# Kernel optimization log

Hardware: AMD Instinct MI355X
Metric: run time of the kernel (lower is better)

## Reference

```python
import jax, jax.numpy as jnp
import numpy as np

B, I, H = 4096, 2048, 2048


def setup_inputs() -> dict:
    key = jax.random.key(0)
    k1, k2, k3, k4, k5 = jax.random.split(key, 5)
    return {
        "x": jax.random.normal(k1, (B, I), dtype=jnp.float32),
        "coefficients": jax.random.normal(k2, (I, H), dtype=jnp.float32) * 0.1,
        "amplitude_an": jax.random.normal(k3, (1, I, H), dtype=jnp.float32) * 0.1,
        "amplitude_bn": jax.random.normal(k4, (1, I, H), dtype=jnp.float32) * 0.1,
        "bias": jax.random.normal(k5, (1, I), dtype=jnp.float32),
    }


def reference(x, coefficients, amplitude_an, amplitude_bn, bias):
    # phase[b,h] = x[b,:] @ coefficients[:,h]  (same matmul done per-sample in torch loop)
    phase = x @ coefficients  # [B, H]
    num_harmonics = coefficients.shape[1]
    # sum over harmonics of an[i,h]*cos(phase[b,h]) + bn[i,h]*sin(phase[b,h])
    gain = (
        jnp.einsum("bh,ih->bi", jnp.cos(phase), amplitude_an[0])
        + jnp.einsum("bh,ih->bi", jnp.sin(phase), amplitude_bn[0])
        + num_harmonics * bias  # bias added per-harmonic before the sum over H
    )
    return gain  # [B, I]
```

## Files before the change

### kernel.cpp

```cpp
#include <hip/hip_runtime.h>
#include <hip/hip_bf16.h>

#define B_DIM 4096
#define I_DIM 2048
#define H_DIM 2048

typedef unsigned char u8;
typedef unsigned short u16;
typedef unsigned int u32;
typedef __attribute__((ext_vector_type(4))) float f32x4;
typedef __attribute__((ext_vector_type(4))) int i32x4;
typedef __attribute__((ext_vector_type(8))) int i32x8;

__device__ __forceinline__ void gload_lds16(const void* g, void* l) {
  __builtin_amdgcn_global_load_lds(
      (const __attribute__((address_space(1))) void*)g,
      (__attribute__((address_space(3))) void*)l, 16, 0, 0);
}

__device__ __forceinline__ u32 f2fp4(float v, float inv_scale) {
  const float a = fabsf(v) * inv_scale;
  u32 m = (u32)(a > 0.25f) + (u32)(a > 0.75f) + (u32)(a > 1.25f) +
          (u32)(a > 1.75f) + (u32)(a > 2.5f) + (u32)(a > 3.5f) + (u32)(a > 5.0f);
  return ((__float_as_uint(v) >> 31) << 3) | m;
}

__global__ void convert_ew(const float* __restrict__ x, const float* __restrict__ an,
                           const float* __restrict__ bn, u16* __restrict__ xf4,
                           u32* __restrict__ ab4) {
  const long NX4 = (long)B_DIM * I_DIM / 4;
  const long NA4 = (long)I_DIM * H_DIM / 4;
  const long total = NX4 + NA4;
  for (long t = (long)blockIdx.x * blockDim.x + threadIdx.x; t < total;
       t += (long)gridDim.x * blockDim.x) {
    if (t < NX4) {
      float4 v = *(const float4*)(x + t * 4);
      u32 b0 = f2fp4(v.x, 1.f) | (f2fp4(v.y, 1.f) << 4);
      u32 b1 = f2fp4(v.z, 1.f) | (f2fp4(v.w, 1.f) << 4);
      xf4[t] = (u16)(b0 | (b1 << 8));
    } else {
      long p = (t - NX4) * 4;
      float4 va = *(const float4*)(an + p);
      float4 vb = *(const float4*)(bn + p);
      u32 b0 = f2fp4(va.x, 8.f) | (f2fp4(vb.x, 8.f) << 4);
      u32 b1 = f2fp4(va.y, 8.f) | (f2fp4(vb.y, 8.f) << 4);
      u32 b2 = f2fp4(va.z, 8.f) | (f2fp4(vb.z, 8.f) << 4);
      u32 b3 = f2fp4(va.w, 8.f) | (f2fp4(vb.w, 8.f) << 4);
      ab4[p >> 2] = b0 | (b1 << 8) | (b2 << 16) | (b3 << 24);
    }
  }
}

__global__ void transpose_conv(const float* __restrict__ c, u16* __restrict__ ct4) {
  __shared__ float tile[32][33];
  const int i0 = blockIdx.y * 32;
  const int h0 = blockIdx.x * 32;
  const int tid = threadIdx.x;
  const int tx = tid & 31;
  const int ty = tid >> 5;
  for (int r = ty; r < 32; r += 8)
    tile[r][tx] = c[(long)(i0 + r) * H_DIM + (h0 + tx)];
  __syncthreads();
  const int hl = tid >> 3;
  const int q = (tid & 7) * 4;
  u32 w = f2fp4(tile[q + 0][hl], 8.f) | (f2fp4(tile[q + 1][hl], 8.f) << 4) |
          (f2fp4(tile[q + 2][hl], 8.f) << 8) | (f2fp4(tile[q + 3][hl], 8.f) << 12);
  ct4[(long)(h0 + hl) * (I_DIM / 4) + ((i0 + q) >> 2)] = (u16)w;
}

__device__ __forceinline__ void stage_tile(const char* Ab, const char* Bb, long kbyte,
                                           long lda, long ldb, char* Adst, char* Bdst,
                                           int tid) {
#pragma unroll
  for (int i = 0; i < 4; ++i) {
    const int o = i * 4096 + tid * 16;
    const int row = o >> 7;
    const int ls = ((((o >> 4) & 7) ^ (row & 7)) << 4);
    gload_lds16(Ab + (long)row * lda + kbyte + ls, Adst + o);
  }
#pragma unroll
  for (int i = 0; i < 4; ++i) {
    const int o = i * 4096 + tid * 16;
    const int row = o >> 7;
    const int ls = ((((o >> 4) & 7) ^ (row & 7)) << 4);
    gload_lds16(Bb + (long)row * ldb + kbyte + ls, Bdst + o);
  }
}

__device__ __forceinline__ i32x4 frag_ld16(const char* S, int row, int slot) {
  return *(const i32x4*)(S + row * 128 + ((slot ^ (row & 7)) << 4));
}

template <int SCALE_A, int SCALE_B>
__device__ __forceinline__ void gemm_kloop_fp4(const char* __restrict__ A,
                                               const char* __restrict__ Bt,
                                               int rowA0, int colB0, long Kbytes,
                                               char* smem, f32x4 acc[4][4]) {
  const int tid = threadIdx.x;
  const int lane = tid & 63;
  const int wid = tid >> 6;
  const int wr = wid >> 1, wc = wid & 1;
  const long lda = Kbytes, ldb = Kbytes;
  const char* Ab = A + (long)rowA0 * lda;
  const char* Bb = Bt + (long)colB0 * ldb;
  const int arow = wr * 64 + (lane & 15);
  const int brow = wc * 64 + (lane & 15);
  const int g = lane >> 4;
  const int nt = (int)(Kbytes >> 7);
  char* AsB = smem;
  char* BsB = smem + 32768;

  stage_tile(Ab, Bb, 0, lda, ldb, AsB, BsB, tid);

  for (int t = 0; t < nt; ++t) {
    const int cur = (t & 1) << 14;
    asm volatile("s_waitcnt vmcnt(0)" ::: "memory");
    __builtin_amdgcn_sched_barrier(0);
    __builtin_amdgcn_s_barrier();
    __builtin_amdgcn_sched_barrier(0);

    i32x8 af[2][4], bfr[2][4];
#pragma unroll
    for (int s = 0; s < 2; ++s)
#pragma unroll
      for (int m = 0; m < 4; ++m) {
        *(i32x4*)&af[s][m]  = frag_ld16(AsB + cur, arow + m * 16, s * 4 + g);
        *(i32x4*)&bfr[s][m] = frag_ld16(BsB + cur, brow + m * 16, s * 4 + g);
      }
    if (t + 1 < nt)
      stage_tile(Ab, Bb, (long)(t + 1) * 128, lda, ldb,
                 AsB + (cur ^ 16384), BsB + (cur ^ 16384), tid);
    __builtin_amdgcn_sched_barrier(0);
    asm volatile("s_waitcnt lgkmcnt(0)" ::: "memory");
    __builtin_amdgcn_sched_barrier(0);

    __builtin_amdgcn_s_setprio(1);
#pragma unroll
    for (int s = 0; s < 2; ++s)
#pragma unroll
      for (int m = 0; m < 4; ++m)
#pragma unroll
        for (int n = 0; n < 4; ++n)
          acc[m][n] = __builtin_amdgcn_mfma_scale_f32_16x16x128_f8f6f4(
              af[s][m], bfr[s][n], acc[m][n], 4, 4, 0, SCALE_A, 0, SCALE_B);
    __builtin_amdgcn_s_setprio(0);
    __builtin_amdgcn_sched_barrier(0);
  }
}

__device__ __forceinline__ void tile_xy(int GX, int& bx, int& by) {
  const int bid = blockIdx.x;
  const int id = (bid & 7) * 64 + (bid >> 3);
  bx = id & (GX - 1);
  by = id / GX;
}

__global__ __launch_bounds__(256) void gemm_phase(const char* __restrict__ xf4,
                                                  const char* __restrict__ ct4,
                                                  u8* __restrict__ cs4) {
  __shared__ __align__(16) char smem[65536];
  int bx, by;
  tile_xy(16, bx, by);
  const int rowA0 = by * 128;
  const int colB0 = bx * 128;
  f32x4 acc[4][4];
#pragma unroll
  for (int m = 0; m < 4; ++m)
#pragma unroll
    for (int n = 0; n < 4; ++n)
#pragma unroll
      for (int j = 0; j < 4; ++j) acc[m][n][j] = 0.0f;

  gemm_kloop_fp4<0x7F7F7F7F, 0x7C7C7C7C>(xf4, ct4, rowA0, colB0, I_DIM / 2, smem, acc);

  const int lane = threadIdx.x & 63;
  const int wid = threadIdx.x >> 6;
  const int wr = wid >> 1, wc = wid & 1;
#pragma unroll
  for (int m = 0; m < 4; ++m) {
#pragma unroll
    for (int n = 0; n < 4; ++n) {
      const int col = colB0 + wc * 64 + n * 16 + (lane & 15);
#pragma unroll
      for (int j = 0; j < 4; ++j) {
        const int row = rowA0 + wr * 64 + m * 16 + (lane >> 4) * 4 + j;
        const float p = acc[m][n][j];
        const u32 b = f2fp4(__cosf(p), 4.f) | (f2fp4(__sinf(p), 4.f) << 4);
        cs4[(long)row * H_DIM + col] = (u8)b;
      }
    }
  }
}

__global__ __launch_bounds__(256) void gemm_gain(const char* __restrict__ cs4,
                                                 const char* __restrict__ ab4,
                                                 const float* __restrict__ bias,
                                                 float* __restrict__ out) {
  __shared__ __align__(16) char smem[65536];
  int bx, by;
  tile_xy(16, bx, by);
  const int rowA0 = by * 128;
  const int colB0 = bx * 128;
  f32x4 acc[4][4];
#pragma unroll
  for (int m = 0; m < 4; ++m)
#pragma unroll
    for (int n = 0; n < 4; ++n)
#pragma unroll
      for (int j = 0; j < 4; ++j) acc[m][n][j] = 0.0f;

  gemm_kloop_fp4<0x7D7D7D7D, 0x7C7C7C7C>(cs4, ab4, rowA0, colB0, H_DIM, smem, acc);

  const int lane = threadIdx.x & 63;
  const int wid = threadIdx.x >> 6;
  const int wr = wid >> 1, wc = wid & 1;
#pragma unroll
  for (int m = 0; m < 4; ++m) {
#pragma unroll
    for (int n = 0; n < 4; ++n) {
      const int col = colB0 + wc * 64 + n * 16 + (lane & 15);
      const float bv = 2048.0f * bias[col];
#pragma unroll
      for (int j = 0; j < 4; ++j) {
        const int row = rowA0 + wr * 64 + m * 16 + (lane >> 4) * 4 + j;
        out[(long)row * I_DIM + col] = acc[m][n][j] + bv;
      }
    }
  }
}

extern "C" void kernel_launch(void* const* d_in, const int* in_sizes, int n_in,
                              void* d_out, int out_size, void* d_ws, size_t ws_size,
                              hipStream_t stream) {
  const float* x     = (const float*)d_in[0];
  const float* coeff = (const float*)d_in[1];
  const float* an    = (const float*)d_in[2];
  const float* bn    = (const float*)d_in[3];
  const float* bias  = (const float*)d_in[4];
  float* out = (float*)d_out;

  char* ws = (char*)d_ws;
  char* xf4 = ws;
  char* ct4 = ws + (4L << 20);
  char* ab4 = ws + (8L << 20);
  u8*  cs4  = (u8*)(ws + (12L << 20));

  convert_ew<<<1024, 256, 0, stream>>>(x, an, bn, (u16*)xf4, (u32*)ab4);
  transpose_conv<<<dim3(H_DIM / 32, I_DIM / 32), 256, 0, stream>>>(coeff, (u16*)ct4);
  gemm_phase<<<512, 256, 0, stream>>>(xf4, ct4, cs4);
  gemm_gain<<<512, 256, 0, stream>>>((const char*)cs4, (const char*)ab4, bias, out);
}
```

Before: 66.40 us.

## Load A fragments directly from global into registers, stage only B in LDS

The FP4 GEMM k-loop now reads A-operand fragments straight from global memory into registers, double-buffered in two register arrays across an unrolled pair of iterations. Only the B tile still goes through LDS via global_load_lds. This halves LDS use per block (64KB to 32KB), which may allow more resident blocks, and removes the A LDS write/read traffic. In exchange, A loads are uncoalesced 16-byte per-lane global reads shared redundantly by the two waves with the same row offset, and register pressure rises.

New measurement: 96.33 us. 1.45x slower.

```diff
diff --git a/kernel.cpp b/kernel.cpp
--- a/kernel.cpp
+++ b/kernel.cpp
@@ -68,16 +68,8 @@
   ct4[(long)(h0 + hl) * (I_DIM / 4) + ((i0 + q) >> 2)] = (u16)w;
 }
 
-__device__ __forceinline__ void stage_tile(const char* Ab, const char* Bb, long kbyte,
-                                           long lda, long ldb, char* Adst, char* Bdst,
-                                           int tid) {
-#pragma unroll
-  for (int i = 0; i < 4; ++i) {
-    const int o = i * 4096 + tid * 16;
-    const int row = o >> 7;
-    const int ls = ((((o >> 4) & 7) ^ (row & 7)) << 4);
-    gload_lds16(Ab + (long)row * lda + kbyte + ls, Adst + o);
-  }
+__device__ __forceinline__ void stageB(const char* Bb, long kbyte, long ldb,
+                                       char* Bdst, int tid) {
 #pragma unroll
   for (int i = 0; i < 4; ++i) {
     const int o = i * 4096 + tid * 16;
@@ -91,60 +83,66 @@
   return *(const i32x4*)(S + row * 128 + ((slot ^ (row & 7)) << 4));
 }
 
-template <int SCALE_A, int SCALE_B>
+#define FS_ITER(CUR, NXT, t)                                                     \
+  {                                                                              \
+    asm volatile("s_waitcnt vmcnt(0)" ::: "memory");                             \
+    __builtin_amdgcn_sched_barrier(0);                                           \
+    __builtin_amdgcn_s_barrier();                                                \
+    __builtin_amdgcn_sched_barrier(0);                                           \
+    const char* Bs = BsB + (((t) & 1) << 14);                                    \
+    i32x8 bfr[8];                                                                \
+    _Pragma("unroll") for (int s = 0; s < 2; ++s)                                \
+      _Pragma("unroll") for (int n = 0; n < 4; ++n)                              \
+        *(i32x4*)&bfr[s * 4 + n] = frag_ld16(Bs, brow + n * 16, s * 4 + g);      \
+    if ((t) + 1 < nt) {                                                          \
+      const long kb = ((long)(t) + 1) * 128;                                     \
+      _Pragma("unroll") for (int s = 0; s < 2; ++s)                              \
+        _Pragma("unroll") for (int m = 0; m < 4; ++m)                            \
+          *(i32x4*)&NXT[s * 4 + m] =                                             \
+              *(const i32x4*)(Arow + (long)m * 16 * lda + kb + (s * 4 + g) * 16);\
+      stageB(Bb, kb, ldb, BsB + ((((t) + 1) & 1) << 14), tid);                   \
+    }                                                                            \
+    __builtin_amdgcn_sched_barrier(0);                                           \
+    asm volatile("s_waitcnt lgkmcnt(0)" ::: "memory");                           \
+    __builtin_amdgcn_sched_barrier(0);                                           \
+    __builtin_amdgcn_s_setprio(1);                                               \
+    _Pragma("unroll") for (int s = 0; s < 2; ++s)                                \
+      _Pragma("unroll") for (int m = 0; m < 4; ++m)                              \
+        _Pragma("unroll") for (int n = 0; n < 4; ++n)                            \
+          acc[m][n] = __builtin_amdgcn_mfma_scale_f32_16x16x128_f8f6f4(          \
+              CUR[s * 4 + m], bfr[s * 4 + n], acc[m][n], 4, 4, 0, SA, 0, SB);    \
+    __builtin_amdgcn_s_setprio(0);                                               \
+    __builtin_amdgcn_sched_barrier(0);                                           \
+  }
+
+template <int SA, int SB>
 __device__ __forceinline__ void gemm_kloop_fp4(const char* __restrict__ A,
                                                const char* __restrict__ Bt,
                                                int rowA0, int colB0, long Kbytes,
-                                               char* smem, f32x4 acc[4][4]) {
+                                               char* BsB, f32x4 acc[4][4]) {
   const int tid = threadIdx.x;
   const int lane = tid & 63;
   const int wid = tid >> 6;
   const int wr = wid >> 1, wc = wid & 1;
   const long lda = Kbytes, ldb = Kbytes;
-  const char* Ab = A + (long)rowA0 * lda;
   const char* Bb = Bt + (long)colB0 * ldb;
-  const int arow = wr * 64 + (lane & 15);
+  const char* Arow = A + (long)(rowA0 + wr * 64 + (lane & 15)) * lda;
   const int brow = wc * 64 + (lane & 15);
   const int g = lane >> 4;
   const int nt = (int)(Kbytes >> 7);
-  char* AsB = smem;
-  char* BsB = smem + 32768;
-
-  stage_tile(Ab, Bb, 0, lda, ldb, AsB, BsB, tid);
-
-  for (int t = 0; t < nt; ++t) {
-    const int cur = (t & 1) << 14;
-    asm volatile("s_waitcnt vmcnt(0)" ::: "memory");
-    __builtin_amdgcn_sched_barrier(0);
-    __builtin_amdgcn_s_barrier();
-    __builtin_amdgcn_sched_barrier(0);
-
-    i32x8 af[2][4], bfr[2][4];
-#pragma unroll
-    for (int s = 0; s < 2; ++s)
-#pragma unroll
-      for (int m = 0; m < 4; ++m) {
-        *(i32x4*)&af[s][m]  = frag_ld16(AsB + cur, arow + m * 16, s * 4 + g);
-        *(i32x4*)&bfr[s][m] = frag_ld16(BsB + cur, brow + m * 16, s * 4 + g);
-      }
-    if (t + 1 < nt)
-      stage_tile(Ab, Bb, (long)(t + 1) * 128, lda, ldb,
-                 AsB + (cur ^ 16384), BsB + (cur ^ 16384), tid);
-    __builtin_amdgcn_sched_barrier(0);
-    asm volatile("s_waitcnt lgkmcnt(0)" ::: "memory");
-    __builtin_amdgcn_sched_barrier(0);
-
-    __builtin_amdgcn_s_setprio(1);
-#pragma unroll
-    for (int s = 0; s < 2; ++s)
-#pragma unroll
-      for (int m = 0; m < 4; ++m)
-#pragma unroll
-        for (int n = 0; n < 4; ++n)
-          acc[m][n] = __builtin_amdgcn_mfma_scale_f32_16x16x128_f8f6f4(
-              af[s][m], bfr[s][n], acc[m][n], 4, 4, 0, SCALE_A, 0, SCALE_B);
-    __builtin_amdgcn_s_setprio(0);
-    __builtin_amdgcn_sched_barrier(0);
+
+  i32x8 afA[8], afB[8];
+#pragma unroll
+  for (int s = 0; s < 2; ++s)
+#pragma unroll
+    for (int m = 0; m < 4; ++m)
+      *(i32x4*)&afA[s * 4 + m] =
+          *(const i32x4*)(Arow + (long)m * 16 * lda + (s * 4 + g) * 16);
+  stageB(Bb, 0, ldb, BsB, tid);
+
+  for (int t = 0; t < nt; t += 2) {
+    FS_ITER(afA, afB, t);
+    FS_ITER(afB, afA, t + 1);
   }
 }
 
@@ -158,7 +156,7 @@
 __global__ __launch_bounds__(256) void gemm_phase(const char* __restrict__ xf4,
                                                   const char* __restrict__ ct4,
                                                   u8* __restrict__ cs4) {
-  __shared__ __align__(16) char smem[65536];
+  __shared__ __align__(16) char smem[32768];
   int bx, by;
   tile_xy(16, bx, by);
   const int rowA0 = by * 128;
@@ -196,7 +194,7 @@
                                                  const char* __restrict__ ab4,
                                                  const float* __restrict__ bias,
                                                  float* __restrict__ out) {
-  __shared__ __align__(16) char smem[65536];
+  __shared__ __align__(16) char smem[32768];
   int bx, by;
   tile_xy(16, bx, by);
   const int rowA0 = by * 128;
```

## Use 128x256 tiles with 8 waves and triple-buffered LDS prefetch

Applied to the files above, without the earlier changes.

Both FP4 GEMM kernels move from 128x128 tiles with 4 waves to 128x256 tiles with 8 waves (512 threads), giving 256 blocks, one per CU. The LDS pipeline goes from double to triple buffering with a prefetch distance of two K-tiles. A partial vmcnt wait lets the next tile's loads stay in flight while the current one is consumed. The aim is to hide global-load latency and reuse each A tile across more columns, at the cost of about 147KB of LDS and one block per CU, which leaves less latency hiding from co-resident blocks.

New measurement: 67.05 us. About the same (+1.0%).

```diff
diff --git a/kernel.cpp b/kernel.cpp
--- a/kernel.cpp
+++ b/kernel.cpp
@@ -68,22 +68,23 @@
   ct4[(long)(h0 + hl) * (I_DIM / 4) + ((i0 + q) >> 2)] = (u16)w;
 }
 
+#define NBUF 49152
+
 __device__ __forceinline__ void stage_tile(const char* Ab, const char* Bb, long kbyte,
-                                           long lda, long ldb, char* Adst, char* Bdst,
-                                           int tid) {
-#pragma unroll
-  for (int i = 0; i < 4; ++i) {
-    const int o = i * 4096 + tid * 16;
+                                           long lda, long ldb, char* buf, int tid) {
+#pragma unroll
+  for (int i = 0; i < 2; ++i) {
+    const int o = i * 8192 + tid * 16;
     const int row = o >> 7;
     const int ls = ((((o >> 4) & 7) ^ (row & 7)) << 4);
-    gload_lds16(Ab + (long)row * lda + kbyte + ls, Adst + o);
+    gload_lds16(Ab + (long)row * lda + kbyte + ls, buf + o);
   }
 #pragma unroll
   for (int i = 0; i < 4; ++i) {
-    const int o = i * 4096 + tid * 16;
+    const int o = i * 8192 + tid * 16;
     const int row = o >> 7;
     const int ls = ((((o >> 4) & 7) ^ (row & 7)) << 4);
-    gload_lds16(Bb + (long)row * ldb + kbyte + ls, Bdst + o);
+    gload_lds16(Bb + (long)row * ldb + kbyte + ls, buf + 16384 + o);
   }
 }
 
@@ -91,7 +92,7 @@
   return *(const i32x4*)(S + row * 128 + ((slot ^ (row & 7)) << 4));
 }
 
-template <int SCALE_A, int SCALE_B>
+template <int SA, int SB>
 __device__ __forceinline__ void gemm_kloop_fp4(const char* __restrict__ A,
                                                const char* __restrict__ Bt,
                                                int rowA0, int colB0, long Kbytes,
@@ -99,7 +100,8 @@
   const int tid = threadIdx.x;
   const int lane = tid & 63;
   const int wid = tid >> 6;
-  const int wr = wid >> 1, wc = wid & 1;
+  const int wr = wid >> 2;
+  const int wc = wid & 3;
   const long lda = Kbytes, ldb = Kbytes;
   const char* Ab = A + (long)rowA0 * lda;
   const char* Bb = Bt + (long)colB0 * ldb;
@@ -107,29 +109,35 @@
   const int brow = wc * 64 + (lane & 15);
   const int g = lane >> 4;
   const int nt = (int)(Kbytes >> 7);
-  char* AsB = smem;
-  char* BsB = smem + 32768;
-
-  stage_tile(Ab, Bb, 0, lda, ldb, AsB, BsB, tid);
+
+  char* b0 = smem;
+  char* b1 = smem + NBUF;
+  char* b2 = smem + 2 * NBUF;
+
+  stage_tile(Ab, Bb, 0, lda, ldb, b0, tid);
+  stage_tile(Ab, Bb, 128, lda, ldb, b1, tid);
 
   for (int t = 0; t < nt; ++t) {
-    const int cur = (t & 1) << 14;
-    asm volatile("s_waitcnt vmcnt(0)" ::: "memory");
+    if (t < nt - 1) asm volatile("s_waitcnt vmcnt(6)" ::: "memory");
+    else            asm volatile("s_waitcnt vmcnt(0)" ::: "memory");
     __builtin_amdgcn_sched_barrier(0);
     __builtin_amdgcn_s_barrier();
     __builtin_amdgcn_sched_barrier(0);
 
-    i32x8 af[2][4], bfr[2][4];
+    i32x8 af[8], bfr[8];
 #pragma unroll
     for (int s = 0; s < 2; ++s)
 #pragma unroll
-      for (int m = 0; m < 4; ++m) {
-        *(i32x4*)&af[s][m]  = frag_ld16(AsB + cur, arow + m * 16, s * 4 + g);
-        *(i32x4*)&bfr[s][m] = frag_ld16(BsB + cur, brow + m * 16, s * 4 + g);
-      }
-    if (t + 1 < nt)
-      stage_tile(Ab, Bb, (long)(t + 1) * 128, lda, ldb,
-                 AsB + (cur ^ 16384), BsB + (cur ^ 16384), tid);
+      for (int m = 0; m < 4; ++m)
+        *(i32x4*)&af[s * 4 + m] = frag_ld16(b0, arow + m * 16, s * 4 + g);
+#pragma unroll
+    for (int s = 0; s < 2; ++s)
+#pragma unroll
+      for (int n = 0; n < 4; ++n)
+        *(i32x4*)&bfr[s * 4 + n] = frag_ld16(b0 + 16384, brow + n * 16, s * 4 + g);
+
+    if (t + 2 < nt)
+      stage_tile(Ab, Bb, (long)(t + 2) * 128, lda, ldb, b2, tid);
     __builtin_amdgcn_sched_barrier(0);
     asm volatile("s_waitcnt lgkmcnt(0)" ::: "memory");
     __builtin_amdgcn_sched_barrier(0);
@@ -142,27 +150,29 @@
 #pragma unroll
         for (int n = 0; n < 4; ++n)
           acc[m][n] = __builtin_amdgcn_mfma_scale_f32_16x16x128_f8f6f4(
-              af[s][m], bfr[s][n], acc[m][n], 4, 4, 0, SCALE_A, 0, SCALE_B);
+              af[s * 4 + m], bfr[s * 4 + n], acc[m][n], 4, 4, 0, SA, 0, SB);
     __builtin_amdgcn_s_setprio(0);
     __builtin_amdgcn_sched_barrier(0);
-  }
-}
-
-__device__ __forceinline__ void tile_xy(int GX, int& bx, int& by) {
+
+    char* tmp = b0; b0 = b1; b1 = b2; b2 = tmp;
+  }
+}
+
+__device__ __forceinline__ void tile_xy(int& bx, int& by) {
   const int bid = blockIdx.x;
-  const int id = (bid & 7) * 64 + (bid >> 3);
-  bx = id & (GX - 1);
-  by = id / GX;
-}
-
-__global__ __launch_bounds__(256) void gemm_phase(const char* __restrict__ xf4,
-                                                  const char* __restrict__ ct4,
-                                                  u8* __restrict__ cs4) {
-  __shared__ __align__(16) char smem[65536];
+  const int id = (bid & 7) * 32 + (bid >> 3);
+  bx = id & 7;
+  by = id >> 3;
+}
+
+__global__ __launch_bounds__(512, 1) void gemm_phase(const char* __restrict__ xf4,
+                                                     const char* __restrict__ ct4,
+                                                     u8* __restrict__ cs4) {
+  __shared__ __align__(16) char smem[3 * NBUF];
   int bx, by;
-  tile_xy(16, bx, by);
+  tile_xy(bx, by);
   const int rowA0 = by * 128;
-  const int colB0 = bx * 128;
+  const int colB0 = bx * 256;
   f32x4 acc[4][4];
 #pragma unroll
   for (int m = 0; m < 4; ++m)
@@ -175,7 +185,7 @@
 
   const int lane = threadIdx.x & 63;
   const int wid = threadIdx.x >> 6;
-  const int wr = wid >> 1, wc = wid & 1;
+  const int wr = wid >> 2, wc = wid & 3;
 #pragma unroll
   for (int m = 0; m < 4; ++m) {
 #pragma unroll
@@ -192,15 +202,15 @@
   }
 }
 
-__global__ __launch_bounds__(256) void gemm_gain(const char* __restrict__ cs4,
-                                                 const char* __restrict__ ab4,
-                                                 const float* __restrict__ bias,
-                                                 float* __restrict__ out) {
-  __shared__ __align__(16) char smem[65536];
+__global__ __launch_bounds__(512, 1) void gemm_gain(const char* __restrict__ cs4,
+                                                    const char* __restrict__ ab4,
+                                                    const float* __restrict__ bias,
+                                                    float* __restrict__ out) {
+  __shared__ __align__(16) char smem[3 * NBUF];
   int bx, by;
-  tile_xy(16, bx, by);
+  tile_xy(bx, by);
   const int rowA0 = by * 128;
-  const int colB0 = bx * 128;
+  const int colB0 = bx * 256;
   f32x4 acc[4][4];
 #pragma unroll
   for (int m = 0; m < 4; ++m)
@@ -213,7 +223,7 @@
 
   const int lane = threadIdx.x & 63;
   const int wid = threadIdx.x >> 6;
-  const int wr = wid >> 1, wc = wid & 1;
+  const int wr = wid >> 2, wc = wid & 3;
 #pragma unroll
   for (int m = 0; m < 4; ++m) {
 #pragma unroll
@@ -247,6 +257,6 @@
 
   convert_ew<<<1024, 256, 0, stream>>>(x, an, bn, (u16*)xf4, (u32*)ab4);
   transpose_conv<<<dim3(H_DIM / 32, I_DIM / 32), 256, 0, stream>>>(coeff, (u16*)ct4);
-  gemm_phase<<<512, 256, 0, stream>>>(xf4, ct4, cs4);
-  gemm_gain<<<512, 256, 0, stream>>>((const char*)cs4, (const char*)ab4, bias, out);
-}
+  gemm_phase<<<256, 512, 0, stream>>>(xf4, ct4, cs4);
+  gemm_gain<<<256, 512, 0, stream>>>((const char*)cs4, (const char*)ab4, bias, out);
+}
```

## Prefetch two K tiles ahead, fuse prep kernels, remap tiles per XCD

Applied to the files above, without the earlier changes.

The FP4 GEMM K-loop now keeps two stages in flight. It waits with vmcnt(8) so the next tile's loads stay outstanding, and uses a second barrier before overwriting the buffer just read. The two preprocessing kernels (elementwise convert and the transpose-convert of coefficients) are merged into one launch that splits the work by block index. Block-to-tile mapping now gives each XCD a contiguous 8x8 tile region to improve L2 reuse. The cost is an extra barrier per iteration and a slightly more complex loop; overlap of global loads with MFMA should improve.

Result: no change. 66.16 us (-0.4%).

```diff
diff --git a/kernel.cpp b/kernel.cpp
--- a/kernel.cpp
+++ b/kernel.cpp
@@ -25,14 +25,33 @@
   return ((__float_as_uint(v) >> 31) << 3) | m;
 }
 
-__global__ void convert_ew(const float* __restrict__ x, const float* __restrict__ an,
-                           const float* __restrict__ bn, u16* __restrict__ xf4,
-                           u32* __restrict__ ab4) {
+__global__ void prep_all(const float* __restrict__ x, const float* __restrict__ coeff,
+                         const float* __restrict__ an, const float* __restrict__ bn,
+                         u16* __restrict__ xf4, u16* __restrict__ ct4,
+                         u32* __restrict__ ab4) {
+  if (blockIdx.x < 4096) {
+    __shared__ float tile[32][33];
+    const int h0 = (blockIdx.x & 63) * 32;
+    const int i0 = (blockIdx.x >> 6) * 32;
+    const int tid = threadIdx.x;
+    const int tx = tid & 31;
+    const int ty = tid >> 5;
+    for (int r = ty; r < 32; r += 8)
+      tile[r][tx] = coeff[(long)(i0 + r) * H_DIM + (h0 + tx)];
+    __syncthreads();
+    const int hl = tid >> 3;
+    const int q = (tid & 7) * 4;
+    u32 w = f2fp4(tile[q + 0][hl], 8.f) | (f2fp4(tile[q + 1][hl], 8.f) << 4) |
+            (f2fp4(tile[q + 2][hl], 8.f) << 8) | (f2fp4(tile[q + 3][hl], 8.f) << 12);
+    ct4[(long)(h0 + hl) * (I_DIM / 4) + ((i0 + q) >> 2)] = (u16)w;
+    return;
+  }
   const long NX4 = (long)B_DIM * I_DIM / 4;
   const long NA4 = (long)I_DIM * H_DIM / 4;
   const long total = NX4 + NA4;
-  for (long t = (long)blockIdx.x * blockDim.x + threadIdx.x; t < total;
-       t += (long)gridDim.x * blockDim.x) {
+  const long stride = (long)1024 * blockDim.x;
+  for (long t = (long)(blockIdx.x - 4096) * blockDim.x + threadIdx.x; t < total;
+       t += stride) {
     if (t < NX4) {
       float4 v = *(const float4*)(x + t * 4);
       u32 b0 = f2fp4(v.x, 1.f) | (f2fp4(v.y, 1.f) << 4);
@@ -51,39 +70,22 @@
   }
 }
 
-__global__ void transpose_conv(const float* __restrict__ c, u16* __restrict__ ct4) {
-  __shared__ float tile[32][33];
-  const int i0 = blockIdx.y * 32;
-  const int h0 = blockIdx.x * 32;
-  const int tid = threadIdx.x;
-  const int tx = tid & 31;
-  const int ty = tid >> 5;
-  for (int r = ty; r < 32; r += 8)
-    tile[r][tx] = c[(long)(i0 + r) * H_DIM + (h0 + tx)];
-  __syncthreads();
-  const int hl = tid >> 3;
-  const int q = (tid & 7) * 4;
-  u32 w = f2fp4(tile[q + 0][hl], 8.f) | (f2fp4(tile[q + 1][hl], 8.f) << 4) |
-          (f2fp4(tile[q + 2][hl], 8.f) << 8) | (f2fp4(tile[q + 3][hl], 8.f) << 12);
-  ct4[(long)(h0 + hl) * (I_DIM / 4) + ((i0 + q) >> 2)] = (u16)w;
-}
-
 __device__ __forceinline__ void stage_tile(const char* Ab, const char* Bb, long kbyte,
-                                           long lda, long ldb, char* Adst, char* Bdst,
+                                           long lda, long ldb, char* AsB, char* BsB,
                                            int tid) {
 #pragma unroll
   for (int i = 0; i < 4; ++i) {
     const int o = i * 4096 + tid * 16;
     const int row = o >> 7;
     const int ls = ((((o >> 4) & 7) ^ (row & 7)) << 4);
-    gload_lds16(Ab + (long)row * lda + kbyte + ls, Adst + o);
+    gload_lds16(Ab + (long)row * lda + kbyte + ls, AsB + o);
   }
 #pragma unroll
   for (int i = 0; i < 4; ++i) {
     const int o = i * 4096 + tid * 16;
     const int row = o >> 7;
     const int ls = ((((o >> 4) & 7) ^ (row & 7)) << 4);
-    gload_lds16(Bb + (long)row * ldb + kbyte + ls, Bdst + o);
+    gload_lds16(Bb + (long)row * ldb + kbyte + ls, BsB + o);
   }
 }
 
@@ -91,7 +93,7 @@
   return *(const i32x4*)(S + row * 128 + ((slot ^ (row & 7)) << 4));
 }
 
-template <int SCALE_A, int SCALE_B>
+template <int SA, int SB>
 __device__ __forceinline__ void gemm_kloop_fp4(const char* __restrict__ A,
                                                const char* __restrict__ Bt,
                                                int rowA0, int colB0, long Kbytes,
@@ -108,31 +110,34 @@
   const int g = lane >> 4;
   const int nt = (int)(Kbytes >> 7);
   char* AsB = smem;
-  char* BsB = smem + 32768;
+  char* BsB = smem + 16384;
 
   stage_tile(Ab, Bb, 0, lda, ldb, AsB, BsB, tid);
+  stage_tile(Ab, Bb, 128, lda, ldb, AsB + 32768, BsB + 32768, tid);
 
   for (int t = 0; t < nt; ++t) {
-    const int cur = (t & 1) << 14;
-    asm volatile("s_waitcnt vmcnt(0)" ::: "memory");
+    const int cur = (t & 1) << 15;
+    if (t < nt - 1) asm volatile("s_waitcnt vmcnt(8)" ::: "memory");
+    else            asm volatile("s_waitcnt vmcnt(0)" ::: "memory");
     __builtin_amdgcn_sched_barrier(0);
     __builtin_amdgcn_s_barrier();
     __builtin_amdgcn_sched_barrier(0);
 
-    i32x8 af[2][4], bfr[2][4];
+    i32x8 af[8], bfr[8];
 #pragma unroll
     for (int s = 0; s < 2; ++s)
 #pragma unroll
       for (int m = 0; m < 4; ++m) {
-        *(i32x4*)&af[s][m]  = frag_ld16(AsB + cur, arow + m * 16, s * 4 + g);
-        *(i32x4*)&bfr[s][m] = frag_ld16(BsB + cur, brow + m * 16, s * 4 + g);
+        *(i32x4*)&af[s * 4 + m]  = frag_ld16(AsB + cur, arow + m * 16, s * 4 + g);
+        *(i32x4*)&bfr[s * 4 + m] = frag_ld16(BsB + cur, brow + m * 16, s * 4 + g);
       }
-    if (t + 1 < nt)
-      stage_tile(Ab, Bb, (long)(t + 1) * 128, lda, ldb,
-                 AsB + (cur ^ 16384), BsB + (cur ^ 16384), tid);
-    __builtin_amdgcn_sched_barrier(0);
     asm volatile("s_waitcnt lgkmcnt(0)" ::: "memory");
     __builtin_amdgcn_sched_barrier(0);
+    __builtin_amdgcn_s_barrier();
+    __builtin_amdgcn_sched_barrier(0);
+
+    if (t + 2 < nt)
+      stage_tile(Ab, Bb, (long)(t + 2) * 128, lda, ldb, AsB + cur, BsB + cur, tid);
 
     __builtin_amdgcn_s_setprio(1);
 #pragma unroll
@@ -142,17 +147,20 @@
 #pragma unroll
         for (int n = 0; n < 4; ++n)
           acc[m][n] = __builtin_amdgcn_mfma_scale_f32_16x16x128_f8f6f4(
-              af[s][m], bfr[s][n], acc[m][n], 4, 4, 0, SCALE_A, 0, SCALE_B);
+              af[s * 4 + m], bfr[s * 4 + n], acc[m][n], 4, 4, 0, SA, 0, SB);
     __builtin_amdgcn_s_setprio(0);
     __builtin_amdgcn_sched_barrier(0);
   }
 }
 
-__device__ __forceinline__ void tile_xy(int GX, int& bx, int& by) {
+__device__ __forceinline__ void tile_xy(int& bx, int& by) {
   const int bid = blockIdx.x;
-  const int id = (bid & 7) * 64 + (bid >> 3);
-  bx = id & (GX - 1);
-  by = id / GX;
+  const int xcd = bid & 7;
+  const int loc = bid >> 3;
+  const int cy = xcd >> 1;
+  const int cx = xcd & 1;
+  by = cy * 8 + (loc >> 3);
+  bx = cx * 8 + (loc & 7);
 }
 
 __global__ __launch_bounds__(256) void gemm_phase(const char* __restrict__ xf4,
@@ -160,7 +168,7 @@
                                                   u8* __restrict__ cs4) {
   __shared__ __align__(16) char smem[65536];
   int bx, by;
-  tile_xy(16, bx, by);
+  tile_xy(bx, by);
   const int rowA0 = by * 128;
   const int colB0 = bx * 128;
   f32x4 acc[4][4];
@@ -198,7 +206,7 @@
                                                  float* __restrict__ out) {
   __shared__ __align__(16) char smem[65536];
   int bx, by;
-  tile_xy(16, bx, by);
+  tile_xy(bx, by);
   const int rowA0 = by * 128;
   const int colB0 = bx * 128;
   f32x4 acc[4][4];
@@ -245,8 +253,8 @@
   char* ab4 = ws + (8L << 20);
   u8*  cs4  = (u8*)(ws + (12L << 20));
 
-  convert_ew<<<1024, 256, 0, stream>>>(x, an, bn, (u16*)xf4, (u32*)ab4);
-  transpose_conv<<<dim3(H_DIM / 32, I_DIM / 32), 256, 0, stream>>>(coeff, (u16*)ct4);
+  prep_all<<<5120, 256, 0, stream>>>(x, coeff, an, bn, (u16*)xf4, (u16*)ct4,
+                                     (u32*)ab4);
   gemm_phase<<<512, 256, 0, stream>>>(xf4, ct4, cs4);
   gemm_gain<<<512, 256, 0, stream>>>((const char*)cs4, (const char*)ab4, bias, out);
 }
```
